# Kernel optimization log

Hardware: AMD Instinct MI355X
Metric: run time of the kernel (lower is better)

Reference implementation:

```python
import jax, jax.numpy as jnp
import numpy as np

B, S, D, H = 4, 2048, 1024, 16
DH = D // H  # attention head size = 64


def setup_inputs() -> dict:
    key = jax.random.key(0)
    ks = jax.random.split(key, 5)
    scale = 1.0 / np.sqrt(D)
    return {
        "hidden_states": jax.random.normal(ks[0], (B, S, D), dtype=jnp.float32),
        "attention_mask": jnp.zeros((B, 1, 1, S), dtype=jnp.float32),
        "Wq": jax.random.normal(ks[1], (D, D), dtype=jnp.float32) * scale,
        "bq": jnp.zeros((D,), dtype=jnp.float32),
        "Wk": jax.random.normal(ks[2], (D, D), dtype=jnp.float32) * scale,
        "bk": jnp.zeros((D,), dtype=jnp.float32),
        "Wv": jax.random.normal(ks[3], (D, D), dtype=jnp.float32) * scale,
        "bv": jnp.zeros((D,), dtype=jnp.float32),
    }


def _heads(x):
    # [B,S,D] -> [B,H,S,DH]
    return x.reshape(B, S, H, DH).transpose(0, 2, 1, 3)


def reference(hidden_states, attention_mask, Wq, bq, Wk, bk, Wv, bv):
    # QKV projections (nn.Linear: x @ W.T + b)
    q = _heads(hidden_states @ Wq.T + bq)
    k = _heads(hidden_states @ Wk.T + bk)
    v = _heads(hidden_states @ Wv.T + bv)
    # scaled dot-product attention, eval mode (no dropout, no head_mask)
    scores = jnp.einsum("bhqd,bhkd->bhqk", q, k) / np.sqrt(DH).astype(np.float32)
    scores = scores + attention_mask  # additive mask broadcast to [B,H,S,S]
    probs = jax.nn.softmax(scores, axis=-1)
    ctx = jnp.einsum("bhqk,bhkd->bhqd", probs, v)
    # [B,H,S,DH] -> [B,S,D]
    return ctx.transpose(0, 2, 1, 3).reshape(B, S, D)
```

## Files before the change

### kernel.cpp

```cpp
#include <hip/hip_runtime.h>

typedef float f32x4 __attribute__((ext_vector_type(4)));
typedef __bf16 bf16x8 __attribute__((ext_vector_type(8)));
typedef unsigned short u16;
typedef unsigned int u32;
typedef u32 u32x4 __attribute__((ext_vector_type(4)));

#define SEQ 2048
#define DMODEL 1024
#define MTOT 8192
#define NQKV 3072
#define LOG2E 1.4426950408889634f
#define C1 0.18033688011112042f

__device__ __forceinline__ u16 f2bf(float f) {
  u32 u = __builtin_bit_cast(u32, f);
  u = (u + 0x7fffu + ((u >> 16) & 1u)) >> 16;
  return (u16)u;
}

__device__ __forceinline__ void gl_lds16(const void* g, void* l) {
  __builtin_amdgcn_global_load_lds(
      (const __attribute__((address_space(1))) u32*)g,
      (__attribute__((address_space(3))) u32*)l, 16, 0, 0);
}

__global__ __launch_bounds__(256) void cvt_kernel(
    const float* __restrict__ X, const float* __restrict__ Wq,
    const float* __restrict__ Wk, const float* __restrict__ Wv,
    const float* __restrict__ mask,
    u16* __restrict__ Xb, u16* __restrict__ Wall, float* __restrict__ mskL) {
  const long NX = (long)MTOT * DMODEL;
  const long NW = (long)DMODEL * DMODEL;
  long i = ((long)blockIdx.x * 256 + threadIdx.x) * 4;
  if (i < NX) {
    float4 v = *reinterpret_cast<const float4*>(X + i);
    u16* dst = Xb + i;
    dst[0] = f2bf(v.x); dst[1] = f2bf(v.y); dst[2] = f2bf(v.z); dst[3] = f2bf(v.w);
  } else {
    long j = i - NX;
    if (j < 3 * NW) {
      long wsel = j >> 20;
      long k = j & (NW - 1);
      const float* src = wsel == 0 ? Wq : (wsel == 1 ? Wk : Wv);
      float4 v = *reinterpret_cast<const float4*>(src + k);
      u16* dst = Wall + j;
      dst[0] = f2bf(v.x); dst[1] = f2bf(v.y); dst[2] = f2bf(v.z); dst[3] = f2bf(v.w);
    } else {
      long jm = j - 3 * NW;
      if (jm < (long)4 * SEQ) {
        float4 v = *reinterpret_cast<const float4*>(mask + jm);
        float4 o = {v.x * LOG2E, v.y * LOG2E, v.z * LOG2E, v.w * LOG2E};
        *reinterpret_cast<float4*>(mskL + jm) = o;
      }
    }
  }
}

__global__ __launch_bounds__(256) void gemm_qkv(
    const u16* __restrict__ A, const u16* __restrict__ Bw,
    const float* __restrict__ bq, const float* __restrict__ bk,
    const float* __restrict__ bv, u16* __restrict__ C) {
  __shared__ __align__(16) u16 As[128 * 32];
  __shared__ __align__(16) u16 Bs[128 * 32];
  const int t = threadIdx.x;
  const int l = t & 63, w = t >> 6;
  const int wr = w >> 1, wc = w & 1;
  const int g16 = l >> 4, l16 = l & 15;
  const long m0 = (long)blockIdx.x * 128;
  const long n0 = (long)blockIdx.y * 128;
  f32x4 acc[4][4] = {};

  const int rA = w * 16 + (l >> 2);
  const int cA = (l & 3) * 8;

  for (int k0 = 0; k0 < DMODEL; k0 += 32) {
#pragma unroll
    for (int is = 0; is < 2; ++is) {
      gl_lds16(A + (m0 + is * 64 + rA) * DMODEL + k0 + cA,
               (char*)As + is * 4096 + w * 1024);
      gl_lds16(Bw + (n0 + is * 64 + rA) * DMODEL + k0 + cA,
               (char*)Bs + is * 4096 + w * 1024);
    }
    __syncthreads();
    bf16x8 af[4], bf[4];
#pragma unroll
    for (int i = 0; i < 4; ++i)
      af[i] = *reinterpret_cast<const bf16x8*>(
          (const char*)As + (wr * 64 + i * 16 + l16) * 64 + g16 * 16);
#pragma unroll
    for (int j = 0; j < 4; ++j)
      bf[j] = *reinterpret_cast<const bf16x8*>(
          (const char*)Bs + (wc * 64 + j * 16 + l16) * 64 + g16 * 16);
#pragma unroll
    for (int i = 0; i < 4; ++i)
#pragma unroll
      for (int j = 0; j < 4; ++j)
        acc[i][j] = __builtin_amdgcn_mfma_f32_16x16x32_bf16(af[i], bf[j], acc[i][j], 0, 0, 0);
    __syncthreads();
  }

#pragma unroll
  for (int j = 0; j < 4; ++j) {
    const long n = n0 + wc * 64 + j * 16 + l16;
    const float bias = n < 1024 ? bq[n] : (n < 2048 ? bk[n - 1024] : bv[n - 2048]);
#pragma unroll
    for (int i = 0; i < 4; ++i) {
      const long m = m0 + wr * 64 + i * 16 + g16 * 4;
#pragma unroll
      for (int r = 0; r < 4; ++r)
        C[(m + r) * NQKV + n] = f2bf(acc[i][j][r] + bias);
    }
  }
}

__global__ __launch_bounds__(256) void attn_kernel(
    const u16* __restrict__ QKV, const float* __restrict__ mskL,
    float* __restrict__ out) {
  __shared__ __align__(16) u16 Ks[2][64 * 64];
  __shared__ __align__(16) u16 Vs[2][64 * 64];
  __shared__ __align__(16) float Mv[2][64];
  __shared__ __align__(16) u16 Pt[4][64 * 18];

  const int qt = blockIdx.x, bh = blockIdx.y;
  const int b = bh >> 4, h = bh & 15;
  const int t = threadIdx.x, l = t & 63, w = t >> 6;
  const int l15 = l & 15, g16 = l >> 4;

  const u16* Qg = QKV + (long)b * SEQ * NQKV + h * 64;
  const u16* Kg = Qg + 1024;
  const u16* Vg = Qg + 2048;
  const float* Mg = mskL + (long)b * SEQ;

  bf16x8 qf[2];
  {
    const long qr = (long)(qt * 64 + w * 16 + l15) * NQKV + g16 * 8;
    qf[0] = *reinterpret_cast<const bf16x8*>(Qg + qr);
    qf[1] = *reinterpret_cast<const bf16x8*>(Qg + qr + 32);
  }

  const int srow = w * 8 + (l >> 3);
  const u16* kp0 = Kg + (long)srow * NQKV + (((l & 7) ^ (l >> 3)) * 8);
  const u16* kp1 = kp0 + (long)32 * NQKV;
  const u16* vp0 = Vg + (long)srow * NQKV + (l & 7) * 8;
  const u16* vp1 = vp0 + (long)32 * NQKV;
  u16* ksDst0 = Ks[0] + w * 512;
  u16* ksDst1 = Ks[1] + w * 512;

  const int vbase = (l & 7) * 1024 + (l >> 3) * 2;

  const int kx0 = (((g16) ^ (l15 & 7)) & 7) << 4;
  const int kx1 = (((4 + g16) ^ (l15 & 7)) & 7) << 4;

  float m_ = -INFINITY, l_ = 0.f;
  f32x4 c_[4] = {};

  {
    u32x4 a0 = *reinterpret_cast<const u32x4*>(vp0);
    u32x4 a1 = *reinterpret_cast<const u32x4*>(vp1);
    gl_lds16(kp0, ksDst0);
    gl_lds16(kp1, ksDst0 + 2048);
    if (t < 16) gl_lds16(Mg + t * 4, Mv[0]);
    char* VsB = (char*)Vs[0];
#pragma unroll
    for (int half = 0; half < 2; ++half) {
      const u32x4 vv = half ? a1 : a0;
      const int cx = (half * 4 + w) ^ (l & 7);
#pragma unroll
      for (int jj = 0; jj < 4; ++jj) {
        const int c0 = (cx ^ (2 * jj)) & 7;
        const u32 pair = vv[jj];
        *(u16*)(VsB + vbase + jj * 256 + (c0 << 4)) = (u16)pair;
        *(u16*)(VsB + vbase + jj * 256 + 128 + ((c0 ^ 1) << 4)) = (u16)(pair >> 16);
      }
    }
  }
  __syncthreads();

  int cb = 0;
  for (int kt = 0; kt < 32; ++kt) {
    u32x4 b0, b1;
    const bool pref = kt < 31;
    if (pref) {
      const long adv = (long)(kt + 1) * 64 * NQKV;
      b0 = *reinterpret_cast<const u32x4*>(vp0 + adv);
      b1 = *reinterpret_cast<const u32x4*>(vp1 + adv);
      u16* kd = (cb ? ksDst0 : ksDst1);
      gl_lds16(kp0 + adv, kd);
      gl_lds16(kp1 + adv, kd + 2048);
      if (t < 16) gl_lds16(Mg + (kt + 1) * 64 + t * 4, Mv[cb ^ 1]);
    }

    const char* KsB = (const char*)Ks[cb];
    f32x4 s4[4] = {};
#pragma unroll
    for (int kt16 = 0; kt16 < 4; ++kt16) {
      const char* rowp = KsB + (kt16 * 16 + l15) * 128;
      bf16x8 k0 = *reinterpret_cast<const bf16x8*>(rowp + kx0);
      bf16x8 k1 = *reinterpret_cast<const bf16x8*>(rowp + kx1);
      s4[kt16] = __builtin_amdgcn_mfma_f32_16x16x32_bf16(k0, qf[0], s4[kt16], 0, 0, 0);
      s4[kt16] = __builtin_amdgcn_mfma_f32_16x16x32_bf16(k1, qf[1], s4[kt16], 0, 0, 0);
    }

    float z[16];
    float mx = -INFINITY;
#pragma unroll
    for (int kt16 = 0; kt16 < 4; ++kt16) {
      f32x4 mv4 = *reinterpret_cast<const f32x4*>(&Mv[cb][kt16 * 16 + g16 * 4]);
#pragma unroll
      for (int r = 0; r < 4; ++r) {
        const float zz = s4[kt16][r] * C1 + mv4[r];
        z[kt16 * 4 + r] = zz;
        mx = fmaxf(mx, zz);
      }
    }
    mx = fmaxf(mx, __shfl_xor(mx, 16, 64));
    mx = fmaxf(mx, __shfl_xor(mx, 32, 64));
    const float mn = fmaxf(m_, mx);
    const float sc = __builtin_amdgcn_exp2f(m_ - mn);
    m_ = mn;
    float rs = 0.f;
#pragma unroll
    for (int i = 0; i < 16; ++i) {
      const float p = __builtin_amdgcn_exp2f(z[i] - mn);
      z[i] = p;
      rs += p;
    }
    rs += __shfl_xor(rs, 16, 64);
    rs += __shfl_xor(rs, 32, 64);
    l_ = l_ * sc + rs;
#pragma unroll
    for (int dt = 0; dt < 4; ++dt) {
      c_[dt][0] *= sc; c_[dt][1] *= sc; c_[dt][2] *= sc; c_[dt][3] *= sc;
    }

    __bf16* PtW = (__bf16*)Pt[w];
#pragma unroll
    for (int kt16 = 0; kt16 < 4; ++kt16)
#pragma unroll
      for (int r = 0; r < 4; ++r)
        PtW[(kt16 * 16 + g16 * 4 + r) * 18 + l15] = (__bf16)z[kt16 * 4 + r];

    const char* VsB = (const char*)Vs[cb];
#pragma unroll
    for (int kh = 0; kh < 2; ++kh) {
      bf16x8 pb;
#pragma unroll
      for (int e = 0; e < 8; ++e)
        pb[e] = PtW[(kh * 32 + g16 * 8 + e) * 18 + l15];
#pragma unroll
      for (int dt = 0; dt < 4; ++dt) {
        const int d = dt * 16 + l15;
        const int fd = ((d >> 3) ^ d) & 7;
        bf16x8 va = *reinterpret_cast<const bf16x8*>(
            VsB + d * 128 + ((((kh * 4 + g16) ^ fd) & 7) << 4));
        c_[dt] = __builtin_amdgcn_mfma_f32_16x16x32_bf16(va, pb, c_[dt], 0, 0, 0);
      }
    }

    if (pref) {
      char* VsN = (char*)Vs[cb ^ 1];
#pragma unroll
      for (int half = 0; half < 2; ++half) {
        const u32x4 vv = half ? b1 : b0;
        const int cx = (half * 4 + w) ^ (l & 7);
#pragma unroll
        for (int jj = 0; jj < 4; ++jj) {
          const int c0 = (cx ^ (2 * jj)) & 7;
          const u32 pair = vv[jj];
          *(u16*)(VsN + vbase + jj * 256 + (c0 << 4)) = (u16)pair;
          *(u16*)(VsN + vbase + jj * 256 + 128 + ((c0 ^ 1) << 4)) = (u16)(pair >> 16);
        }
      }
    }
    __syncthreads();
    cb ^= 1;
  }

  const float inv = 1.0f / l_;
  const long orow = ((long)b * SEQ + qt * 64 + w * 16 + l15) * DMODEL + h * 64;
#pragma unroll
  for (int dt = 0; dt < 4; ++dt) {
    f32x4 o = {c_[dt][0] * inv, c_[dt][1] * inv, c_[dt][2] * inv, c_[dt][3] * inv};
    *reinterpret_cast<f32x4*>(out + orow + dt * 16 + g16 * 4) = o;
  }
}

extern "C" void kernel_launch(void* const* d_in, const int* in_sizes, int n_in,
                              void* d_out, int out_size, void* d_ws, size_t ws_size,
                              hipStream_t stream) {
  const float* X    = (const float*)d_in[0];
  const float* mask = (const float*)d_in[1];
  const float* Wq   = (const float*)d_in[2];
  const float* bq   = (const float*)d_in[3];
  const float* Wk   = (const float*)d_in[4];
  const float* bk   = (const float*)d_in[5];
  const float* Wv   = (const float*)d_in[6];
  const float* bv   = (const float*)d_in[7];
  float* out = (float*)d_out;

  char* ws = (char*)d_ws;
  u16* Xb    = (u16*)ws;
  u16* Wall  = (u16*)(ws + (16ull << 20));
  u16* QKV   = (u16*)(ws + (16ull << 20) + (6ull << 20));
  float* mskL = (float*)(ws + (70ull << 20));

  cvt_kernel<<<11272, 256, 0, stream>>>(X, Wq, Wk, Wv, mask, Xb, Wall, mskL);
  gemm_qkv<<<dim3(64, 24), 256, 0, stream>>>(Xb, Wall, bq, bk, bv, QKV);
  attn_kernel<<<dim3(32, 64), 256, 0, stream>>>(QKV, mskL, out);
}
```

Before: 343.6 us.

## Split QKV GEMM, write V transposed, stream V via direct LDS loads

Splits the fused QKV projection into a Q/K GEMM with packed row-major stores and a V GEMM that writes V transposed per head. The attention kernel can then load V straight into shared memory with async global-to-LDS copies instead of register loads and scattered 16-bit stores. It also adds a lazy softmax rescale that skips the rescale when the running max grows by at most 8 in log2 units, a vectorized P staging layout, and MFMA priority hints. The costs are an extra kernel launch and the transposed-store pattern in the V epilogue, and the skipped rescale slightly changes the numerics.

```diff
diff --git a/kernel.cpp b/kernel.cpp
--- a/kernel.cpp
+++ b/kernel.cpp
@@ -2,22 +2,15 @@
 
 typedef float f32x4 __attribute__((ext_vector_type(4)));
 typedef __bf16 bf16x8 __attribute__((ext_vector_type(8)));
+typedef __bf16 bf16x4 __attribute__((ext_vector_type(4)));
 typedef unsigned short u16;
 typedef unsigned int u32;
-typedef u32 u32x4 __attribute__((ext_vector_type(4)));
 
 #define SEQ 2048
 #define DMODEL 1024
 #define MTOT 8192
-#define NQKV 3072
 #define LOG2E 1.4426950408889634f
 #define C1 0.18033688011112042f
-
-__device__ __forceinline__ u16 f2bf(float f) {
-  u32 u = __builtin_bit_cast(u32, f);
-  u = (u + 0x7fffu + ((u >> 16) & 1u)) >> 16;
-  return (u16)u;
-}
 
 __device__ __forceinline__ void gl_lds16(const void* g, void* l) {
   __builtin_amdgcn_global_load_lds(
@@ -35,8 +28,8 @@
   long i = ((long)blockIdx.x * 256 + threadIdx.x) * 4;
   if (i < NX) {
     float4 v = *reinterpret_cast<const float4*>(X + i);
-    u16* dst = Xb + i;
-    dst[0] = f2bf(v.x); dst[1] = f2bf(v.y); dst[2] = f2bf(v.z); dst[3] = f2bf(v.w);
+    bf16x4 o = {(__bf16)v.x, (__bf16)v.y, (__bf16)v.z, (__bf16)v.w};
+    *reinterpret_cast<bf16x4*>(Xb + i) = o;
   } else {
     long j = i - NX;
     if (j < 3 * NW) {
@@ -44,8 +37,8 @@
       long k = j & (NW - 1);
       const float* src = wsel == 0 ? Wq : (wsel == 1 ? Wk : Wv);
       float4 v = *reinterpret_cast<const float4*>(src + k);
-      u16* dst = Wall + j;
-      dst[0] = f2bf(v.x); dst[1] = f2bf(v.y); dst[2] = f2bf(v.z); dst[3] = f2bf(v.w);
+      bf16x4 o = {(__bf16)v.x, (__bf16)v.y, (__bf16)v.z, (__bf16)v.w};
+      *reinterpret_cast<bf16x4*>(Wall + j) = o;
     } else {
       long jm = j - 3 * NW;
       if (jm < (long)4 * SEQ) {
@@ -57,16 +50,16 @@
   }
 }
 
-__global__ __launch_bounds__(256) void gemm_qkv(
+__global__ __launch_bounds__(256) void gemm_qk(
     const u16* __restrict__ A, const u16* __restrict__ Bw,
     const float* __restrict__ bq, const float* __restrict__ bk,
-    const float* __restrict__ bv, u16* __restrict__ C) {
+    u16* __restrict__ Qb, u16* __restrict__ Kb) {
   __shared__ __align__(16) u16 As[128 * 32];
   __shared__ __align__(16) u16 Bs[128 * 32];
   const int t = threadIdx.x;
   const int l = t & 63, w = t >> 6;
   const int wr = w >> 1, wc = w & 1;
-  const int g16 = l >> 4, l16 = l & 15;
+  const int g16 = l >> 4, l15 = l & 15;
   const long m0 = (long)blockIdx.x * 128;
   const long n0 = (long)blockIdx.y * 128;
   f32x4 acc[4][4] = {};
@@ -87,11 +80,71 @@
 #pragma unroll
     for (int i = 0; i < 4; ++i)
       af[i] = *reinterpret_cast<const bf16x8*>(
-          (const char*)As + (wr * 64 + i * 16 + l16) * 64 + g16 * 16);
+          (const char*)As + (wr * 64 + i * 16 + l15) * 64 + g16 * 16);
 #pragma unroll
     for (int j = 0; j < 4; ++j)
       bf[j] = *reinterpret_cast<const bf16x8*>(
-          (const char*)Bs + (wc * 64 + j * 16 + l16) * 64 + g16 * 16);
+          (const char*)Bs + (wc * 64 + j * 16 + l15) * 64 + g16 * 16);
+#pragma unroll
+    for (int i = 0; i < 4; ++i)
+#pragma unroll
+      for (int j = 0; j < 4; ++j)
+        acc[i][j] = __builtin_amdgcn_mfma_f32_16x16x32_bf16(bf[j], af[i], acc[i][j], 0, 0, 0);
+    __syncthreads();
+  }
+
+  const bool isQ = n0 < 1024;
+  const float* bias = isQ ? bq : bk;
+  u16* Cb = isQ ? Qb : Kb;
+  const long nb = isQ ? n0 : n0 - 1024;
+#pragma unroll
+  for (int j = 0; j < 4; ++j) {
+    const int nq = wc * 64 + j * 16 + g16 * 4;
+    f32x4 bv4 = *reinterpret_cast<const f32x4*>(bias + nb + nq);
+#pragma unroll
+    for (int i = 0; i < 4; ++i) {
+      const long m = m0 + wr * 64 + i * 16 + l15;
+      bf16x4 pk = {(__bf16)(acc[i][j][0] + bv4[0]), (__bf16)(acc[i][j][1] + bv4[1]),
+                   (__bf16)(acc[i][j][2] + bv4[2]), (__bf16)(acc[i][j][3] + bv4[3])};
+      *reinterpret_cast<bf16x4*>(Cb + m * 1024 + nb + nq) = pk;
+    }
+  }
+}
+
+__global__ __launch_bounds__(256) void gemm_v(
+    const u16* __restrict__ A, const u16* __restrict__ Bw,
+    const float* __restrict__ bv, u16* __restrict__ Vt) {
+  __shared__ __align__(16) u16 As[128 * 32];
+  __shared__ __align__(16) u16 Bs[128 * 32];
+  const int t = threadIdx.x;
+  const int l = t & 63, w = t >> 6;
+  const int wr = w >> 1, wc = w & 1;
+  const int g16 = l >> 4, l15 = l & 15;
+  const long m0 = (long)blockIdx.x * 128;
+  const long n0 = (long)blockIdx.y * 128;
+  f32x4 acc[4][4] = {};
+
+  const int rA = w * 16 + (l >> 2);
+  const int cA = (l & 3) * 8;
+
+  for (int k0 = 0; k0 < DMODEL; k0 += 32) {
+#pragma unroll
+    for (int is = 0; is < 2; ++is) {
+      gl_lds16(A + (m0 + is * 64 + rA) * DMODEL + k0 + cA,
+               (char*)As + is * 4096 + w * 1024);
+      gl_lds16(Bw + (n0 + is * 64 + rA) * DMODEL + k0 + cA,
+               (char*)Bs + is * 4096 + w * 1024);
+    }
+    __syncthreads();
+    bf16x8 af[4], bf[4];
+#pragma unroll
+    for (int i = 0; i < 4; ++i)
+      af[i] = *reinterpret_cast<const bf16x8*>(
+          (const char*)As + (wr * 64 + i * 16 + l15) * 64 + g16 * 16);
+#pragma unroll
+    for (int j = 0; j < 4; ++j)
+      bf[j] = *reinterpret_cast<const bf16x8*>(
+          (const char*)Bs + (wc * 64 + j * 16 + l15) * 64 + g16 * 16);
 #pragma unroll
     for (int i = 0; i < 4; ++i)
 #pragma unroll
@@ -102,105 +155,83 @@
 
 #pragma unroll
   for (int j = 0; j < 4; ++j) {
-    const long n = n0 + wc * 64 + j * 16 + l16;
-    const float bias = n < 1024 ? bq[n] : (n < 2048 ? bk[n - 1024] : bv[n - 2048]);
+    const int dg = (int)n0 + wc * 64 + j * 16 + l15;
+    const float bias = bv[dg];
+    const int h = dg >> 6, dd = dg & 63;
 #pragma unroll
     for (int i = 0; i < 4; ++i) {
       const long m = m0 + wr * 64 + i * 16 + g16 * 4;
-#pragma unroll
-      for (int r = 0; r < 4; ++r)
-        C[(m + r) * NQKV + n] = f2bf(acc[i][j][r] + bias);
+      const long b = m >> 11, s = m & 2047;
+      bf16x4 pk = {(__bf16)(acc[i][j][0] + bias), (__bf16)(acc[i][j][1] + bias),
+                   (__bf16)(acc[i][j][2] + bias), (__bf16)(acc[i][j][3] + bias)};
+      *reinterpret_cast<bf16x4*>(Vt + ((b * 16 + h) * 64 + dd) * 2048 + s) = pk;
     }
   }
 }
 
 __global__ __launch_bounds__(256) void attn_kernel(
-    const u16* __restrict__ QKV, const float* __restrict__ mskL,
+    const u16* __restrict__ Qb, const u16* __restrict__ Kb,
+    const u16* __restrict__ Vt, const float* __restrict__ mskL,
     float* __restrict__ out) {
   __shared__ __align__(16) u16 Ks[2][64 * 64];
   __shared__ __align__(16) u16 Vs[2][64 * 64];
   __shared__ __align__(16) float Mv[2][64];
-  __shared__ __align__(16) u16 Pt[4][64 * 18];
+  __shared__ __align__(16) u16 Pt[4][16 * 72];
 
   const int qt = blockIdx.x, bh = blockIdx.y;
   const int b = bh >> 4, h = bh & 15;
   const int t = threadIdx.x, l = t & 63, w = t >> 6;
   const int l15 = l & 15, g16 = l >> 4;
 
-  const u16* Qg = QKV + (long)b * SEQ * NQKV + h * 64;
-  const u16* Kg = Qg + 1024;
-  const u16* Vg = Qg + 2048;
+  bf16x8 qf0, qf1;
+  {
+    const u16* Qg = Qb + ((long)b * SEQ + qt * 64 + w * 16 + l15) * 1024 + h * 64 + g16 * 8;
+    qf0 = *reinterpret_cast<const bf16x8*>(Qg);
+    qf1 = *reinterpret_cast<const bf16x8*>(Qg + 32);
+  }
+
+  const int swz = ((l & 7) ^ (l >> 3)) * 8;
+  const u16* kp0 = Kb + ((long)b * SEQ + w * 8 + (l >> 3)) * 1024 + h * 64 + swz;
+  const u16* kp1 = kp0 + (long)32 * 1024;
+  const u16* vp0 = Vt + ((long)bh * 64 + w * 16 + (l >> 3)) * 2048 + swz;
+  const u16* vp1 = vp0 + (long)8 * 2048;
   const float* Mg = mskL + (long)b * SEQ;
-
-  bf16x8 qf[2];
-  {
-    const long qr = (long)(qt * 64 + w * 16 + l15) * NQKV + g16 * 8;
-    qf[0] = *reinterpret_cast<const bf16x8*>(Qg + qr);
-    qf[1] = *reinterpret_cast<const bf16x8*>(Qg + qr + 32);
-  }
-
-  const int srow = w * 8 + (l >> 3);
-  const u16* kp0 = Kg + (long)srow * NQKV + (((l & 7) ^ (l >> 3)) * 8);
-  const u16* kp1 = kp0 + (long)32 * NQKV;
-  const u16* vp0 = Vg + (long)srow * NQKV + (l & 7) * 8;
-  const u16* vp1 = vp0 + (long)32 * NQKV;
-  u16* ksDst0 = Ks[0] + w * 512;
-  u16* ksDst1 = Ks[1] + w * 512;
-
-  const int vbase = (l & 7) * 1024 + (l >> 3) * 2;
-
-  const int kx0 = (((g16) ^ (l15 & 7)) & 7) << 4;
-  const int kx1 = (((4 + g16) ^ (l15 & 7)) & 7) << 4;
 
   float m_ = -INFINITY, l_ = 0.f;
   f32x4 c_[4] = {};
 
-  {
-    u32x4 a0 = *reinterpret_cast<const u32x4*>(vp0);
-    u32x4 a1 = *reinterpret_cast<const u32x4*>(vp1);
-    gl_lds16(kp0, ksDst0);
-    gl_lds16(kp1, ksDst0 + 2048);
-    if (t < 16) gl_lds16(Mg + t * 4, Mv[0]);
-    char* VsB = (char*)Vs[0];
-#pragma unroll
-    for (int half = 0; half < 2; ++half) {
-      const u32x4 vv = half ? a1 : a0;
-      const int cx = (half * 4 + w) ^ (l & 7);
-#pragma unroll
-      for (int jj = 0; jj < 4; ++jj) {
-        const int c0 = (cx ^ (2 * jj)) & 7;
-        const u32 pair = vv[jj];
-        *(u16*)(VsB + vbase + jj * 256 + (c0 << 4)) = (u16)pair;
-        *(u16*)(VsB + vbase + jj * 256 + 128 + ((c0 ^ 1) << 4)) = (u16)(pair >> 16);
-      }
-    }
-  }
+#define STAGE(buf, kt)                                              \
+  {                                                                 \
+    const long ka = (long)(kt) * 64 * 1024;                         \
+    const long va = (long)(kt) * 64;                                \
+    gl_lds16(kp0 + ka, Ks[buf] + w * 512);                          \
+    gl_lds16(kp1 + ka, Ks[buf] + w * 512 + 2048);                   \
+    gl_lds16(vp0 + va, Vs[buf] + w * 1024);                         \
+    gl_lds16(vp1 + va, Vs[buf] + w * 1024 + 512);                   \
+    if (t < 16) gl_lds16(Mg + (kt) * 64 + t * 4, Mv[buf]);          \
+  }
+
+  STAGE(0, 0);
   __syncthreads();
 
   int cb = 0;
   for (int kt = 0; kt < 32; ++kt) {
-    u32x4 b0, b1;
-    const bool pref = kt < 31;
-    if (pref) {
-      const long adv = (long)(kt + 1) * 64 * NQKV;
-      b0 = *reinterpret_cast<const u32x4*>(vp0 + adv);
-      b1 = *reinterpret_cast<const u32x4*>(vp1 + adv);
-      u16* kd = (cb ? ksDst0 : ksDst1);
-      gl_lds16(kp0 + adv, kd);
-      gl_lds16(kp1 + adv, kd + 2048);
-      if (t < 16) gl_lds16(Mg + (kt + 1) * 64 + t * 4, Mv[cb ^ 1]);
-    }
+    if (kt < 31) STAGE(cb ^ 1, kt + 1);
 
     const char* KsB = (const char*)Ks[cb];
+    const int kx0 = ((g16 ^ (l15 & 7)) & 7) << 4;
+    const int kx1 = (((4 + g16) ^ (l15 & 7)) & 7) << 4;
     f32x4 s4[4] = {};
+    __builtin_amdgcn_s_setprio(1);
 #pragma unroll
     for (int kt16 = 0; kt16 < 4; ++kt16) {
       const char* rowp = KsB + (kt16 * 16 + l15) * 128;
       bf16x8 k0 = *reinterpret_cast<const bf16x8*>(rowp + kx0);
       bf16x8 k1 = *reinterpret_cast<const bf16x8*>(rowp + kx1);
-      s4[kt16] = __builtin_amdgcn_mfma_f32_16x16x32_bf16(k0, qf[0], s4[kt16], 0, 0, 0);
-      s4[kt16] = __builtin_amdgcn_mfma_f32_16x16x32_bf16(k1, qf[1], s4[kt16], 0, 0, 0);
-    }
+      s4[kt16] = __builtin_amdgcn_mfma_f32_16x16x32_bf16(k0, qf0, s4[kt16], 0, 0, 0);
+      s4[kt16] = __builtin_amdgcn_mfma_f32_16x16x32_bf16(k1, qf1, s4[kt16], 0, 0, 0);
+    }
+    __builtin_amdgcn_s_setprio(0);
 
     float z[16];
     float mx = -INFINITY;
@@ -216,63 +247,51 @@
     }
     mx = fmaxf(mx, __shfl_xor(mx, 16, 64));
     mx = fmaxf(mx, __shfl_xor(mx, 32, 64));
-    const float mn = fmaxf(m_, mx);
-    const float sc = __builtin_amdgcn_exp2f(m_ - mn);
-    m_ = mn;
+    if (!__all(mx <= m_ + 8.0f)) {
+      const float mn = fmaxf(m_, mx);
+      const float sc = __builtin_amdgcn_exp2f(m_ - mn);
+      m_ = mn;
+      l_ *= sc;
+#pragma unroll
+      for (int dt = 0; dt < 4; ++dt) {
+        c_[dt][0] *= sc; c_[dt][1] *= sc; c_[dt][2] *= sc; c_[dt][3] *= sc;
+      }
+    }
     float rs = 0.f;
 #pragma unroll
     for (int i = 0; i < 16; ++i) {
-      const float p = __builtin_amdgcn_exp2f(z[i] - mn);
+      const float p = __builtin_amdgcn_exp2f(z[i] - m_);
       z[i] = p;
       rs += p;
     }
     rs += __shfl_xor(rs, 16, 64);
     rs += __shfl_xor(rs, 32, 64);
-    l_ = l_ * sc + rs;
-#pragma unroll
-    for (int dt = 0; dt < 4; ++dt) {
-      c_[dt][0] *= sc; c_[dt][1] *= sc; c_[dt][2] *= sc; c_[dt][3] *= sc;
-    }
-
-    __bf16* PtW = (__bf16*)Pt[w];
-#pragma unroll
-    for (int kt16 = 0; kt16 < 4; ++kt16)
-#pragma unroll
-      for (int r = 0; r < 4; ++r)
-        PtW[(kt16 * 16 + g16 * 4 + r) * 18 + l15] = (__bf16)z[kt16 * 4 + r];
+    l_ += rs;
+
+    u16* Pw = Pt[w];
+#pragma unroll
+    for (int kt16 = 0; kt16 < 4; ++kt16) {
+      bf16x4 pv = {(__bf16)z[kt16 * 4 + 0], (__bf16)z[kt16 * 4 + 1],
+                   (__bf16)z[kt16 * 4 + 2], (__bf16)z[kt16 * 4 + 3]};
+      *reinterpret_cast<bf16x4*>(Pw + l15 * 72 + kt16 * 16 + g16 * 4) = pv;
+    }
+    asm volatile("s_waitcnt lgkmcnt(0)" ::: "memory");
+    __builtin_amdgcn_sched_barrier(0);
 
     const char* VsB = (const char*)Vs[cb];
+    __builtin_amdgcn_s_setprio(1);
 #pragma unroll
     for (int kh = 0; kh < 2; ++kh) {
-      bf16x8 pb;
-#pragma unroll
-      for (int e = 0; e < 8; ++e)
-        pb[e] = PtW[(kh * 32 + g16 * 8 + e) * 18 + l15];
+      bf16x8 pb = *reinterpret_cast<const bf16x8*>(Pw + l15 * 72 + kh * 32 + g16 * 8);
 #pragma unroll
       for (int dt = 0; dt < 4; ++dt) {
         const int d = dt * 16 + l15;
-        const int fd = ((d >> 3) ^ d) & 7;
         bf16x8 va = *reinterpret_cast<const bf16x8*>(
-            VsB + d * 128 + ((((kh * 4 + g16) ^ fd) & 7) << 4));
+            VsB + d * 128 + ((((kh * 4 + g16) ^ (d & 7)) & 7) << 4));
         c_[dt] = __builtin_amdgcn_mfma_f32_16x16x32_bf16(va, pb, c_[dt], 0, 0, 0);
       }
     }
-
-    if (pref) {
-      char* VsN = (char*)Vs[cb ^ 1];
-#pragma unroll
-      for (int half = 0; half < 2; ++half) {
-        const u32x4 vv = half ? b1 : b0;
-        const int cx = (half * 4 + w) ^ (l & 7);
-#pragma unroll
-        for (int jj = 0; jj < 4; ++jj) {
-          const int c0 = (cx ^ (2 * jj)) & 7;
-          const u32 pair = vv[jj];
-          *(u16*)(VsN + vbase + jj * 256 + (c0 << 4)) = (u16)pair;
-          *(u16*)(VsN + vbase + jj * 256 + 128 + ((c0 ^ 1) << 4)) = (u16)(pair >> 16);
-        }
-      }
-    }
+    __builtin_amdgcn_s_setprio(0);
     __syncthreads();
     cb ^= 1;
   }
@@ -302,10 +321,13 @@
   char* ws = (char*)d_ws;
   u16* Xb    = (u16*)ws;
   u16* Wall  = (u16*)(ws + (16ull << 20));
-  u16* QKV   = (u16*)(ws + (16ull << 20) + (6ull << 20));
+  u16* Qb    = (u16*)(ws + (22ull << 20));
+  u16* Kb    = (u16*)(ws + (38ull << 20));
+  u16* Vt    = (u16*)(ws + (54ull << 20));
   float* mskL = (float*)(ws + (70ull << 20));
 
   cvt_kernel<<<11272, 256, 0, stream>>>(X, Wq, Wk, Wv, mask, Xb, Wall, mskL);
-  gemm_qkv<<<dim3(64, 24), 256, 0, stream>>>(Xb, Wall, bq, bk, bv, QKV);
-  attn_kernel<<<dim3(32, 64), 256, 0, stream>>>(QKV, mskL, out);
-}
+  gemm_qk<<<dim3(64, 16), 256, 0, stream>>>(Xb, Wall, bq, bk, Qb, Kb);
+  gemm_v<<<dim3(64, 8), 256, 0, stream>>>(Xb, Wall + (long)2048 * 1024, bv, Vt);
+  attn_kernel<<<dim3(32, 64), 256, 0, stream>>>(Qb, Kb, Vt, mskL, out);
+}
```

After: 322.7 us. 1.06x faster.
